# Performance work log

Hardware: AMD Instinct MI355X
Metric: run time of the kernel (lower is better)

Reference implementation:

```python
import jax, jax.numpy as jnp
import numpy as np

B, S, D, H, DQ, DV = 4, 2048, 1024, 16, 64, 64

def setup_inputs() -> dict:
    key = jax.random.key(0)
    ks = jax.random.split(key, 11)
    s_in = 1.0 / np.sqrt(D)
    s_o = 1.0 / np.sqrt(H * DV)
    return {
        "query": jax.random.normal(ks[0], (B, S, D), jnp.float32),
        "key":   jax.random.normal(ks[1], (B, S, D), jnp.float32),
        "value": jax.random.normal(ks[2], (B, S, D), jnp.float32),
        "Wq_w": jax.random.normal(ks[3], (D, H * DQ), jnp.float32) * s_in,
        "Wq_b": jax.random.normal(ks[4], (H * DQ,), jnp.float32) * s_in,
        "Wk_w": jax.random.normal(ks[5], (D, H * DQ), jnp.float32) * s_in,
        "Wk_b": jax.random.normal(ks[6], (H * DQ,), jnp.float32) * s_in,
        "Wv_w": jax.random.normal(ks[7], (D, H * DV), jnp.float32) * s_in,
        "Wv_b": jax.random.normal(ks[8], (H * DV,), jnp.float32) * s_in,
        "Wo_w": jax.random.normal(ks[9], (H * DV, D), jnp.float32) * s_o,
        "Wo_b": jax.random.normal(ks[10], (D,), jnp.float32) * s_o,
    }

def reference(query, key, value, Wq_w, Wq_b, Wk_w, Wk_b, Wv_w, Wv_b, Wo_w, Wo_b):
    b, s, d = query.shape
    # chunk(h, dim=-1) + cat(dim=0) == split last dim into (h, dq) per-head slices
    q = (query @ Wq_w + Wq_b).reshape(b, s, H, DQ)  # bshq
    k = (key   @ Wk_w + Wk_b).reshape(b, s, H, DQ)
    v = (value @ Wv_w + Wv_b).reshape(b, s, H, DV)
    # NOTE: source scales by sqrt(K) where K = seq_len (query.shape[1])
    scores = jnp.einsum("bshq,bthq->bhst", q, k) / jnp.sqrt(jnp.float32(s))
    attn = jax.nn.softmax(scores, axis=-1)          # (b, h, s, s)
    out = jnp.einsum("bhst,bthv->bshv", attn, v).reshape(b, s, H * DV)
    return out @ Wo_w + Wo_b
```

## Files before the change

kernel.cpp:

```cpp
#include <hip/hip_runtime.h>
#include <hip/hip_bf16.h>
#include <cstdint>


typedef __attribute__((ext_vector_type(4))) float f32x4;
typedef __attribute__((ext_vector_type(8))) short bf16x8;

#define GLB const __attribute__((address_space(1))) void*
#define LDS __attribute__((address_space(3))) void*

__device__ __forceinline__ ushort f2bf(float f) {
    uint32_t u = __builtin_bit_cast(uint32_t, f);
    u += 0x7fffu + ((u >> 16) & 1u);
    return (ushort)(u >> 16);
}

__device__ __forceinline__ uint32_t cvt_pk_bf16(float lo, float hi) {
    uint32_t r;
    asm("v_cvt_pk_bf16_f32 %0, %1, %2" : "=v"(r) : "v"(lo), "v"(hi));
    return r;
}

__global__ void prep(const float* __restrict__ qf, const float* __restrict__ kf,
                     const float* __restrict__ vf,
                     const float* __restrict__ w0, const float* __restrict__ w1,
                     const float* __restrict__ w2, const float* __restrict__ w3,
                     ushort* __restrict__ oq, ushort* __restrict__ ok,
                     ushort* __restrict__ ov,
                     ushort* __restrict__ t0, ushort* __restrict__ t1,
                     ushort* __restrict__ t2, ushort* __restrict__ t3, int n8) {
    __shared__ float tile[64][65];
    const int y = blockIdx.y;
    if (y < 3) {
        const float* in = y == 0 ? qf : y == 1 ? kf : vf;
        ushort* out     = y == 0 ? oq : y == 1 ? ok : ov;
        for (int i = blockIdx.x * blockDim.x + threadIdx.x; i < n8; i += gridDim.x * blockDim.x) {
            const float4 a = reinterpret_cast<const float4*>(in)[2 * i];
            const float4 b = reinterpret_cast<const float4*>(in)[2 * i + 1];
            uint4 o;
            o.x = cvt_pk_bf16(a.x, a.y);
            o.y = cvt_pk_bf16(a.z, a.w);
            o.z = cvt_pk_bf16(b.x, b.y);
            o.w = cvt_pk_bf16(b.z, b.w);
            reinterpret_cast<uint4*>(out)[i] = o;
        }
    } else {
        const int x = blockIdx.x;
        const int wz = x >> 8, wy = (x >> 4) & 15, wx = x & 15;
        const float* in = wz == 0 ? w0 : wz == 1 ? w1 : wz == 2 ? w2 : w3;
        ushort* out     = wz == 0 ? t0 : wz == 1 ? t1 : wz == 2 ? t2 : t3;
        const int tx = threadIdx.x & 63, ty = threadIdx.x >> 6;
        const int nb = wx * 64, kb = wy * 64;
#pragma unroll
        for (int i = ty; i < 64; i += 4)
            tile[i][tx] = in[(size_t)(kb + i) * 1024 + nb + tx];
        __syncthreads();
#pragma unroll
        for (int i = ty; i < 64; i += 4)
            out[(size_t)(nb + i) * 1024 + kb + tx] = f2bf(tile[tx][i]);
    }
}

#define GEMM_STAGE(A_, BT_, k0, Ad, Bd)                                             \
    _Pragma("unroll")                                                               \
    for (int jj = 0; jj < 2; ++jj) {                                                \
        const int t = jj * 256 + tid;                                               \
        const int lo = (jj * 256 + (tid & ~63)) * 8;                                \
        __builtin_amdgcn_global_load_lds((GLB)(A_  + (size_t)(mb + (t >> 2)) * 1024 + (k0) + (t & 3) * 8), (LDS)(Ad + lo), 16, 0, 0); \
        __builtin_amdgcn_global_load_lds((GLB)(BT_ + (size_t)(nb + (t >> 2)) * 1024 + (k0) + (t & 3) * 8), (LDS)(Bd + lo), 16, 0, 0); \
    }

#define GEMM_BODY(A_, BT_)                                                          \
    f32x4 acc[4][4] = {};                                                           \
    GEMM_STAGE(A_, BT_, 0, As[0], Bs[0])                                            \
    __syncthreads();                                                                \
    for (int k0 = 0; k0 < 1024; k0 += 32) {                                         \
        const int cur = (k0 >> 5) & 1;                                              \
        if (k0 + 32 < 1024) {                                                       \
            GEMM_STAGE(A_, BT_, k0 + 32, As[cur ^ 1], Bs[cur ^ 1])                  \
        }                                                                           \
        bf16x8 af[4], bfr[4];                                                       \
        _Pragma("unroll")                                                           \
        for (int i = 0; i < 4; ++i) {                                               \
            af[i]  = *(const bf16x8*)&As[cur][(wr * 64 + i * 16 + r) * 32 + g * 8]; \
            bfr[i] = *(const bf16x8*)&Bs[cur][(wc * 64 + i * 16 + r) * 32 + g * 8]; \
        }                                                                           \
        __builtin_amdgcn_s_setprio(1);                                              \
        _Pragma("unroll")                                                           \
        for (int mi = 0; mi < 4; ++mi)                                              \
            _Pragma("unroll")                                                       \
            for (int ni = 0; ni < 4; ++ni)                                          \
                acc[mi][ni] = __builtin_amdgcn_mfma_f32_16x16x32_bf16(af[mi], bfr[ni], acc[mi][ni], 0, 0, 0); \
        __builtin_amdgcn_s_setprio(0);                                              \
        __syncthreads();                                                            \
    }

__global__ __launch_bounds__(256) void gemm_qkv(const ushort* __restrict__ qb,
                                                const ushort* __restrict__ kb,
                                                const ushort* __restrict__ vb,
                                                const ushort* __restrict__ WqT,
                                                const ushort* __restrict__ WkT,
                                                const ushort* __restrict__ WvT,
                                                const float* __restrict__ Wq_b,
                                                const float* __restrict__ Wk_b,
                                                const float* __restrict__ Wv_b,
                                                ushort* __restrict__ Qp,
                                                ushort* __restrict__ Kp,
                                                ushort* __restrict__ Vt,
                                                float qscale) {
    __shared__ ushort As[2][128 * 32];
    __shared__ ushort Bs[2][128 * 32];
    const int tid = threadIdx.x;
    const int lane = tid & 63;
    const int wave = tid >> 6, wr = wave >> 1, wc = wave & 1;
    const int r = lane & 15, g = lane >> 4;
    const int proj = blockIdx.y;
    const int id = blockIdx.x;
    const int xcd = id & 7, j = id >> 3;
    const int bx = j >> 3, by = xcd * 8 + (j & 7);
    const int mb = by * 128, nb = bx * 128;

    const ushort* A    = proj == 0 ? qb : proj == 1 ? kb : vb;
    const ushort* BT   = proj == 0 ? WqT : proj == 1 ? WkT : WvT;
    const float*  bias = proj == 0 ? Wq_b : proj == 1 ? Wk_b : Wv_b;

    GEMM_BODY(A, BT)

    const float oscale = proj == 0 ? qscale : 1.0f;
#pragma unroll
    for (int ni = 0; ni < 4; ++ni) {
        const int col = nb + wc * 64 + ni * 16 + r;
        const float bv = bias[col];
#pragma unroll
        for (int mi = 0; mi < 4; ++mi) {
            const int m0 = mb + wr * 64 + mi * 16 + g * 4;
            if (proj < 2) {
                ushort* C = proj == 0 ? Qp : Kp;
#pragma unroll
                for (int i = 0; i < 4; ++i)
                    C[(size_t)(m0 + i) * 1024 + col] = f2bf((acc[mi][ni][i] + bv) * oscale);
            } else {
                const int b = m0 >> 11, s = m0 & 2047;
                const int h = col >> 6, dv = col & 63;
                ushort4 o;
                o.x = f2bf(acc[mi][ni][0] + bv);
                o.y = f2bf(acc[mi][ni][1] + bv);
                o.z = f2bf(acc[mi][ni][2] + bv);
                o.w = f2bf(acc[mi][ni][3] + bv);
                *(ushort4*)&Vt[(((size_t)(b * 16 + h) * 64 + dv) << 11) + s] = o;
            }
        }
    }
}

__global__ __launch_bounds__(256) void gemm_out(const ushort* __restrict__ A_,
                                                const ushort* __restrict__ BT_,
                                                const float* __restrict__ bias,
                                                float* __restrict__ Cf) {
    __shared__ ushort As[2][128 * 32];
    __shared__ ushort Bs[2][128 * 32];
    const int tid = threadIdx.x;
    const int lane = tid & 63;
    const int wave = tid >> 6, wr = wave >> 1, wc = wave & 1;
    const int r = lane & 15, g = lane >> 4;
    const int id = blockIdx.x;
    const int xcd = id & 7, j = id >> 3;
    const int bx = j >> 3, by = xcd * 8 + (j & 7);
    const int mb = by * 128, nb = bx * 128;

    GEMM_BODY(A_, BT_)

#pragma unroll
    for (int ni = 0; ni < 4; ++ni) {
        const int col = nb + wc * 64 + ni * 16 + r;
        const float bv = bias[col];
#pragma unroll
        for (int mi = 0; mi < 4; ++mi) {
            const int m0 = mb + wr * 64 + mi * 16 + g * 4;
#pragma unroll
            for (int i = 0; i < 4; ++i)
                Cf[(size_t)(m0 + i) * 1024 + col] = acc[mi][ni][i] + bv;
        }
    }
}

__global__ __launch_bounds__(512, 4) void attn_kernel(const ushort* __restrict__ Qp,
                                                      const ushort* __restrict__ Kp,
                                                      const ushort* __restrict__ Vt,
                                                      ushort* __restrict__ AO) {
    const int tid = threadIdx.x;
    const int lane = tid & 63, wave = tid >> 6;
    const int r = lane & 15, g = lane >> 4;
    const int id = blockIdx.x;
    const int xcd = id & 7, j = id >> 3;
    const int qt = j & 7;
    const int grp = xcd * 8 + (j >> 3);
    const int h = grp & 15, b = grp >> 4;
    const int qbase = qt * 256 + wave * 32;

    const ushort* Qh = Qp + (size_t)b * 2048 * 1024 + h * 64;
    const ushort* Kh = Kp + (size_t)b * 2048 * 1024 + h * 64;
    const ushort* Vh = Vt + ((size_t)(b * 16 + h)) * 64 * 2048;

    __shared__ ushort Ks[2][64 * 64];
    __shared__ ushort Vs[2][64 * 64];
    __shared__ ushort Pl[8][32 * 64];
    ushort* Pw = (ushort*)Pl[wave];

    const int srow = tid >> 3;
    const int scb  = ((tid & 7) * 16) ^ ((srow & 7) << 4);
    const int wlds = wave * 512;
    const ushort* gKn = Kh + (size_t)srow * 1024 + (scb >> 1) + 64 * 1024;
    const ushort* gVn = Vh + (size_t)srow * 2048 + (scb >> 1) + 64;

    int fro[4][2];
#pragma unroll
    for (int tf = 0; tf < 4; ++tf)
#pragma unroll
        for (int kc = 0; kc < 2; ++kc) {
            const int row = tf * 16 + r;
            fro[tf][kc] = row * 128 + ((kc * 64 + g * 16) ^ ((row & 7) << 4));
        }
    int pwo[2][4], pro[2][2];
#pragma unroll
    for (int gg = 0; gg < 2; ++gg) {
        const int row = gg * 16 + r;
#pragma unroll
        for (int tf = 0; tf < 4; ++tf)
            pwo[gg][tf] = row * 128 + ((tf * 32 + g * 8) ^ ((row & 7) << 4));
#pragma unroll
        for (int kc = 0; kc < 2; ++kc)
            pro[gg][kc] = row * 128 + ((kc * 64 + g * 16) ^ ((row & 7) << 4));
    }

    bf16x8 qf[2][2];
#pragma unroll
    for (int gg = 0; gg < 2; ++gg)
#pragma unroll
        for (int kc = 0; kc < 2; ++kc)
            qf[gg][kc] = *(const bf16x8*)&Qh[(size_t)(qbase + gg * 16 + r) * 1024 + kc * 32 + g * 8];

    f32x4 oacc[2][4] = {};
    float ell[2] = {0.f, 0.f};

    __builtin_amdgcn_global_load_lds((GLB)(gKn - 64 * 1024), (LDS)(Ks[0] + wlds), 16, 0, 0);
    __builtin_amdgcn_global_load_lds((GLB)(gVn - 64), (LDS)(Vs[0] + wlds), 16, 0, 0);
    __syncthreads();

    for (int t0 = 0; t0 < 2048; t0 += 64) {
        const int cur = (t0 >> 6) & 1;
        if (t0 + 64 < 2048) {
            __builtin_amdgcn_global_load_lds((GLB)gKn, (LDS)(Ks[cur ^ 1] + wlds), 16, 0, 0);
            __builtin_amdgcn_global_load_lds((GLB)gVn, (LDS)(Vs[cur ^ 1] + wlds), 16, 0, 0);
            gKn += 64 * 1024;
            gVn += 64;
        }

        const char* Kb = (const char*)Ks[cur];
        bf16x8 kf[4][2];
#pragma unroll
        for (int tf = 0; tf < 4; ++tf)
#pragma unroll
            for (int kc = 0; kc < 2; ++kc)
                kf[tf][kc] = *(const bf16x8*)(Kb + fro[tf][kc]);

        f32x4 st[2][4] = {};
        __builtin_amdgcn_s_setprio(1);
#pragma unroll
        for (int gg = 0; gg < 2; ++gg)
#pragma unroll
            for (int tf = 0; tf < 4; ++tf)
#pragma unroll
                for (int kc = 0; kc < 2; ++kc)
                    st[gg][tf] = __builtin_amdgcn_mfma_f32_16x16x32_bf16(kf[tf][kc], qf[gg][kc], st[gg][tf], 0, 0, 0);
        __builtin_amdgcn_s_setprio(0);

#pragma unroll
        for (int gg = 0; gg < 2; ++gg) {
            float psum = 0.f;
#pragma unroll
            for (int tf = 0; tf < 4; ++tf) {
                const float p0 = __builtin_amdgcn_exp2f(st[gg][tf][0]);
                const float p1 = __builtin_amdgcn_exp2f(st[gg][tf][1]);
                const float p2 = __builtin_amdgcn_exp2f(st[gg][tf][2]);
                const float p3 = __builtin_amdgcn_exp2f(st[gg][tf][3]);
                psum += (p0 + p1) + (p2 + p3);
                uint2 pk;
                pk.x = cvt_pk_bf16(p0, p1);
                pk.y = cvt_pk_bf16(p2, p3);
                *(uint2*)((char*)Pw + pwo[gg][tf]) = pk;
            }
            psum += __shfl_xor(psum, 16);
            psum += __shfl_xor(psum, 32);
            ell[gg] += psum;
        }

        const char* Vb = (const char*)Vs[cur];
        bf16x8 vf[4][2];
#pragma unroll
        for (int mf = 0; mf < 4; ++mf)
#pragma unroll
            for (int kc = 0; kc < 2; ++kc)
                vf[mf][kc] = *(const bf16x8*)(Vb + fro[mf][kc]);

        __builtin_amdgcn_s_setprio(1);
#pragma unroll
        for (int gg = 0; gg < 2; ++gg) {
#pragma unroll
            for (int kc = 0; kc < 2; ++kc) {
                const bf16x8 pf = *(const bf16x8*)((const char*)Pw + pro[gg][kc]);
#pragma unroll
                for (int mf = 0; mf < 4; ++mf)
                    oacc[gg][mf] = __builtin_amdgcn_mfma_f32_16x16x32_bf16(vf[mf][kc], pf, oacc[gg][mf], 0, 0, 0);
            }
        }
        __builtin_amdgcn_s_setprio(0);

        __syncthreads();
    }

#pragma unroll
    for (int gg = 0; gg < 2; ++gg) {
        const float inv = 1.f / ell[gg];
        const int q = qbase + gg * 16 + r;
#pragma unroll
        for (int mf = 0; mf < 4; ++mf) {
            ushort4 o;
            o.x = f2bf(oacc[gg][mf][0] * inv);
            o.y = f2bf(oacc[gg][mf][1] * inv);
            o.z = f2bf(oacc[gg][mf][2] * inv);
            o.w = f2bf(oacc[gg][mf][3] * inv);
            *(ushort4*)&AO[(size_t)(b * 2048 + q) * 1024 + h * 64 + mf * 16 + g * 4] = o;
        }
    }
}

extern "C" void kernel_launch(void* const* d_in, const int* in_sizes, int n_in,
                              void* d_out, int out_size, void* d_ws, size_t ws_size,
                              hipStream_t stream) {
    const float* q_f  = (const float*)d_in[0];
    const float* k_f  = (const float*)d_in[1];
    const float* v_f  = (const float*)d_in[2];
    const float* Wq_w = (const float*)d_in[3];
    const float* Wq_b = (const float*)d_in[4];
    const float* Wk_w = (const float*)d_in[5];
    const float* Wk_b = (const float*)d_in[6];
    const float* Wv_w = (const float*)d_in[7];
    const float* Wv_b = (const float*)d_in[8];
    const float* Wo_w = (const float*)d_in[9];
    const float* Wo_b = (const float*)d_in[10];
    float* out = (float*)d_out;
    char* ws = (char*)d_ws;

    const size_t MB = 1ull << 20;
    ushort* qb  = (ushort*)(ws);
    ushort* kb  = (ushort*)(ws + 16 * MB);
    ushort* vb  = (ushort*)(ws + 32 * MB);
    ushort* WqT = (ushort*)(ws + 48 * MB);
    ushort* WkT = (ushort*)(ws + 50 * MB);
    ushort* WvT = (ushort*)(ws + 52 * MB);
    ushort* WoT = (ushort*)(ws + 54 * MB);
    ushort* Qp  = (ushort*)(ws + 56 * MB);
    ushort* Kp  = (ushort*)(ws + 72 * MB);
    ushort* Vt  = (ushort*)(ws + 88 * MB);
    ushort* AO  = qb;

    const int n8 = (4 * 2048 * 1024) / 8;
    prep<<<dim3(1024, 4), 256, 0, stream>>>(q_f, k_f, v_f, Wq_w, Wk_w, Wv_w, Wo_w,
                                            qb, kb, vb, WqT, WkT, WvT, WoT, n8);

    constexpr float QSCALE = (float)(1.4426950408889634 / 45.254833995939045);

    gemm_qkv<<<dim3(512, 3), 256, 0, stream>>>(qb, kb, vb, WqT, WkT, WvT,
                                               Wq_b, Wk_b, Wv_b, Qp, Kp, Vt, QSCALE);

    attn_kernel<<<512, 512, 0, stream>>>(Qp, Kp, Vt, AO);

    gemm_out<<<512, 256, 0, stream>>>(AO, WoT, Wo_b, out);
}
```

Baseline: 204.2 us.

## Switch attention to 32x32x16 MFMA and keep P in registers via permlane swap

Rewrites the attention inner loop to use 32x32x16 bf16 MFMAs instead of 16x16x32, with each lane owning one query row. The softmax probabilities are packed to bf16 and redistributed with permlane32_swap so they feed the PV MFMA straight from registers, removing the per-wave LDS round trip for P and the LDS scratch it occupied. Row sums now need only one cross-half shuffle at the end instead of shuffles every tile. In exchange it relies on the permlane32_swap instruction (gfx950) and a fragment layout mapping that must be exactly right for correctness.

```diff
diff --git a/kernel.cpp b/kernel.cpp
--- a/kernel.cpp
+++ b/kernel.cpp
@@ -4,6 +4,7 @@
 
 
 typedef __attribute__((ext_vector_type(4))) float f32x4;
+typedef __attribute__((ext_vector_type(16))) float f32x16;
 typedef __attribute__((ext_vector_type(8))) short bf16x8;
 
 #define GLB const __attribute__((address_space(1))) void*
@@ -19,6 +20,12 @@
     uint32_t r;
     asm("v_cvt_pk_bf16_f32 %0, %1, %2" : "=v"(r) : "v"(lo), "v"(hi));
     return r;
+}
+
+__device__ __forceinline__ void plswap(uint32_t& a, uint32_t& b) {
+    auto r = __builtin_amdgcn_permlane32_swap(a, b, false, false);
+    a = r[0];
+    b = r[1];
 }
 
 __global__ void prep(const float* __restrict__ qf, const float* __restrict__ kf,
@@ -190,13 +197,13 @@
                                                       ushort* __restrict__ AO) {
     const int tid = threadIdx.x;
     const int lane = tid & 63, wave = tid >> 6;
-    const int r = lane & 15, g = lane >> 4;
+    const int l31 = lane & 31, hl = lane >> 5;
     const int id = blockIdx.x;
     const int xcd = id & 7, j = id >> 3;
     const int qt = j & 7;
     const int grp = xcd * 8 + (j >> 3);
     const int h = grp & 15, b = grp >> 4;
-    const int qbase = qt * 256 + wave * 32;
+    const int qrow = qt * 256 + wave * 32 + l31;
 
     const ushort* Qh = Qp + (size_t)b * 2048 * 1024 + h * 64;
     const ushort* Kh = Kp + (size_t)b * 2048 * 1024 + h * 64;
@@ -204,8 +211,6 @@
 
     __shared__ ushort Ks[2][64 * 64];
     __shared__ ushort Vs[2][64 * 64];
-    __shared__ ushort Pl[8][32 * 64];
-    ushort* Pw = (ushort*)Pl[wave];
 
     const int srow = tid >> 3;
     const int scb  = ((tid & 7) * 16) ^ ((srow & 7) << 4);
@@ -213,35 +218,22 @@
     const ushort* gKn = Kh + (size_t)srow * 1024 + (scb >> 1) + 64 * 1024;
     const ushort* gVn = Vh + (size_t)srow * 2048 + (scb >> 1) + 64;
 
-    int fro[4][2];
-#pragma unroll
-    for (int tf = 0; tf < 4; ++tf)
-#pragma unroll
-        for (int kc = 0; kc < 2; ++kc) {
-            const int row = tf * 16 + r;
-            fro[tf][kc] = row * 128 + ((kc * 64 + g * 16) ^ ((row & 7) << 4));
-        }
-    int pwo[2][4], pro[2][2];
-#pragma unroll
-    for (int gg = 0; gg < 2; ++gg) {
-        const int row = gg * 16 + r;
-#pragma unroll
-        for (int tf = 0; tf < 4; ++tf)
-            pwo[gg][tf] = row * 128 + ((tf * 32 + g * 8) ^ ((row & 7) << 4));
-#pragma unroll
-        for (int kc = 0; kc < 2; ++kc)
-            pro[gg][kc] = row * 128 + ((kc * 64 + g * 16) ^ ((row & 7) << 4));
-    }
-
-    bf16x8 qf[2][2];
-#pragma unroll
-    for (int gg = 0; gg < 2; ++gg)
-#pragma unroll
-        for (int kc = 0; kc < 2; ++kc)
-            qf[gg][kc] = *(const bf16x8*)&Qh[(size_t)(qbase + gg * 16 + r) * 1024 + kc * 32 + g * 8];
-
-    f32x4 oacc[2][4] = {};
-    float ell[2] = {0.f, 0.f};
+    int fro2[2][4];
+#pragma unroll
+    for (int t2 = 0; t2 < 2; ++t2)
+#pragma unroll
+        for (int c = 0; c < 4; ++c) {
+            const int row = t2 * 32 + l31;
+            fro2[t2][c] = row * 128 + ((c * 32 + hl * 16) ^ ((row & 7) << 4));
+        }
+
+    bf16x8 qf[4];
+#pragma unroll
+    for (int kq = 0; kq < 4; ++kq)
+        qf[kq] = *(const bf16x8*)&Qh[(size_t)qrow * 1024 + kq * 16 + hl * 8];
+
+    f32x16 o2[2] = {};
+    float ell = 0.f;
 
     __builtin_amdgcn_global_load_lds((GLB)(gKn - 64 * 1024), (LDS)(Ks[0] + wlds), 16, 0, 0);
     __builtin_amdgcn_global_load_lds((GLB)(gVn - 64), (LDS)(Vs[0] + wlds), 16, 0, 0);
@@ -257,82 +249,71 @@
         }
 
         const char* Kb = (const char*)Ks[cur];
-        bf16x8 kf[4][2];
-#pragma unroll
-        for (int tf = 0; tf < 4; ++tf)
-#pragma unroll
-            for (int kc = 0; kc < 2; ++kc)
-                kf[tf][kc] = *(const bf16x8*)(Kb + fro[tf][kc]);
-
-        f32x4 st[2][4] = {};
+        const char* Vb = (const char*)Vs[cur];
+
+        bf16x8 pfr[2][2];
+#pragma unroll
+        for (int th = 0; th < 2; ++th) {
+            f32x16 s = {};
+            __builtin_amdgcn_s_setprio(1);
+#pragma unroll
+            for (int kq = 0; kq < 4; ++kq) {
+                const bf16x8 kf = *(const bf16x8*)(Kb + fro2[th][kq]);
+                s = __builtin_amdgcn_mfma_f32_32x32x16_bf16(kf, qf[kq], s, 0, 0, 0);
+            }
+            __builtin_amdgcn_s_setprio(0);
+
+            float p[16];
+#pragma unroll
+            for (int i = 0; i < 16; ++i) p[i] = __builtin_amdgcn_exp2f(s[i]);
+            ell += ((p[0] + p[1]) + (p[2] + p[3])) + ((p[4] + p[5]) + (p[6] + p[7]))
+                 + ((p[8] + p[9]) + (p[10] + p[11])) + ((p[12] + p[13]) + (p[14] + p[15]));
+
+            uint32_t w0 = cvt_pk_bf16(p[0], p[1]);
+            uint32_t w1 = cvt_pk_bf16(p[2], p[3]);
+            uint32_t w2 = cvt_pk_bf16(p[4], p[5]);
+            uint32_t w3 = cvt_pk_bf16(p[6], p[7]);
+            plswap(w0, w2);
+            plswap(w1, w3);
+            uint4 f0; f0.x = w0; f0.y = w1; f0.z = w2; f0.w = w3;
+            pfr[th][0] = __builtin_bit_cast(bf16x8, f0);
+            uint32_t w4 = cvt_pk_bf16(p[8], p[9]);
+            uint32_t w5 = cvt_pk_bf16(p[10], p[11]);
+            uint32_t w6 = cvt_pk_bf16(p[12], p[13]);
+            uint32_t w7 = cvt_pk_bf16(p[14], p[15]);
+            plswap(w4, w6);
+            plswap(w5, w7);
+            uint4 f1; f1.x = w4; f1.y = w5; f1.z = w6; f1.w = w7;
+            pfr[th][1] = __builtin_bit_cast(bf16x8, f1);
+        }
+
         __builtin_amdgcn_s_setprio(1);
 #pragma unroll
-        for (int gg = 0; gg < 2; ++gg)
-#pragma unroll
-            for (int tf = 0; tf < 4; ++tf)
-#pragma unroll
-                for (int kc = 0; kc < 2; ++kc)
-                    st[gg][tf] = __builtin_amdgcn_mfma_f32_16x16x32_bf16(kf[tf][kc], qf[gg][kc], st[gg][tf], 0, 0, 0);
+        for (int vh = 0; vh < 2; ++vh)
+#pragma unroll
+            for (int kt = 0; kt < 4; ++kt) {
+                const bf16x8 vf = *(const bf16x8*)(Vb + fro2[vh][kt]);
+                o2[vh] = __builtin_amdgcn_mfma_f32_32x32x16_bf16(vf, pfr[kt >> 1][kt & 1], o2[vh], 0, 0, 0);
+            }
         __builtin_amdgcn_s_setprio(0);
 
-#pragma unroll
-        for (int gg = 0; gg < 2; ++gg) {
-            float psum = 0.f;
-#pragma unroll
-            for (int tf = 0; tf < 4; ++tf) {
-                const float p0 = __builtin_amdgcn_exp2f(st[gg][tf][0]);
-                const float p1 = __builtin_amdgcn_exp2f(st[gg][tf][1]);
-                const float p2 = __builtin_amdgcn_exp2f(st[gg][tf][2]);
-                const float p3 = __builtin_amdgcn_exp2f(st[gg][tf][3]);
-                psum += (p0 + p1) + (p2 + p3);
-                uint2 pk;
-                pk.x = cvt_pk_bf16(p0, p1);
-                pk.y = cvt_pk_bf16(p2, p3);
-                *(uint2*)((char*)Pw + pwo[gg][tf]) = pk;
-            }
-            psum += __shfl_xor(psum, 16);
-            psum += __shfl_xor(psum, 32);
-            ell[gg] += psum;
-        }
-
-        const char* Vb = (const char*)Vs[cur];
-        bf16x8 vf[4][2];
-#pragma unroll
-        for (int mf = 0; mf < 4; ++mf)
-#pragma unroll
-            for (int kc = 0; kc < 2; ++kc)
-                vf[mf][kc] = *(const bf16x8*)(Vb + fro[mf][kc]);
-
-        __builtin_amdgcn_s_setprio(1);
-#pragma unroll
-        for (int gg = 0; gg < 2; ++gg) {
-#pragma unroll
-            for (int kc = 0; kc < 2; ++kc) {
-                const bf16x8 pf = *(const bf16x8*)((const char*)Pw + pro[gg][kc]);
-#pragma unroll
-                for (int mf = 0; mf < 4; ++mf)
-                    oacc[gg][mf] = __builtin_amdgcn_mfma_f32_16x16x32_bf16(vf[mf][kc], pf, oacc[gg][mf], 0, 0, 0);
-            }
-        }
-        __builtin_amdgcn_s_setprio(0);
-
         __syncthreads();
     }
 
-#pragma unroll
-    for (int gg = 0; gg < 2; ++gg) {
-        const float inv = 1.f / ell[gg];
-        const int q = qbase + gg * 16 + r;
-#pragma unroll
-        for (int mf = 0; mf < 4; ++mf) {
+    ell += __shfl_xor(ell, 32);
+    const float inv = 1.f / ell;
+#pragma unroll
+    for (int vh = 0; vh < 2; ++vh)
+#pragma unroll
+        for (int g4 = 0; g4 < 4; ++g4) {
             ushort4 o;
-            o.x = f2bf(oacc[gg][mf][0] * inv);
-            o.y = f2bf(oacc[gg][mf][1] * inv);
-            o.z = f2bf(oacc[gg][mf][2] * inv);
-            o.w = f2bf(oacc[gg][mf][3] * inv);
-            *(ushort4*)&AO[(size_t)(b * 2048 + q) * 1024 + h * 64 + mf * 16 + g * 4] = o;
-        }
-    }
+            o.x = f2bf(o2[vh][4 * g4 + 0] * inv);
+            o.y = f2bf(o2[vh][4 * g4 + 1] * inv);
+            o.z = f2bf(o2[vh][4 * g4 + 2] * inv);
+            o.w = f2bf(o2[vh][4 * g4 + 3] * inv);
+            const int dvb = 8 * g4 + 4 * hl + 32 * vh;
+            *(ushort4*)&AO[(size_t)(b * 2048 + qrow) * 1024 + h * 64 + dvb] = o;
+        }
 }
 
 extern "C" void kernel_launch(void* const* d_in, const int* in_sizes, int n_in,
```

New measurement: 201.2 us. About the same (-1.5%).
